# Optimization experiments

Hardware: AMD Instinct MI355X
Metric: run time of the kernel (lower is better)

## Reference

```python
import jax, jax.numpy as jnp
import numpy as np

N, E, IN = 50000, 800000, 64
HC, FC1, FC2, FC3, OUT = 96, 256, 128, 64, 8
EPS = 1e-5


def setup_inputs() -> dict:
    key = jax.random.key(0)
    ks = jax.random.split(key, 24)
    def lin(k, fi, fo):
        # kaiming_uniform with relu gain: bound = sqrt(6/fi)
        b = np.sqrt(6.0 / fi)
        return jax.random.uniform(k, (fi, fo), jnp.float32, -b, b)
    inp = {
        'x': jax.random.normal(ks[0], (N, IN), jnp.float32),
        'edge_index': jax.random.randint(ks[1], (2, E), 0, N, jnp.int64),
        'w1': lin(ks[2], IN, HC), 'b1': jnp.zeros((HC,), jnp.float32),
        'g1': jax.random.uniform(ks[3], (HC,), jnp.float32, 0.5, 1.5), 'be1': jax.random.normal(ks[4], (HC,), jnp.float32) * 0.1,
        'w2': lin(ks[5], HC, HC), 'b2': jnp.zeros((HC,), jnp.float32),
        'g2': jax.random.uniform(ks[6], (HC,), jnp.float32, 0.5, 1.5), 'be2': jax.random.normal(ks[7], (HC,), jnp.float32) * 0.1,
        'w3': lin(ks[8], HC, HC), 'b3': jnp.zeros((HC,), jnp.float32),
        'g3': jax.random.uniform(ks[9], (HC,), jnp.float32, 0.5, 1.5), 'be3': jax.random.normal(ks[10], (HC,), jnp.float32) * 0.1,
        'lw1': lin(ks[11], HC, FC1), 'lb1': jnp.zeros((FC1,), jnp.float32),
        'lw2': lin(ks[12], FC1, FC2), 'lb2': jnp.zeros((FC2,), jnp.float32),
        'lw3': lin(ks[13], FC2, FC3), 'lb3': jnp.zeros((FC3,), jnp.float32),
        'lw4': lin(ks[14], FC3, OUT), 'lb4': jnp.zeros((OUT,), jnp.float32),
    }
    return inp


def _gcn(x, w, b, src, dst, norm):
    # GCNConv: out[dst] += norm_e * (x @ w)[src]; then + bias
    h = x @ w
    msg = h[src] * norm[:, None]
    return jax.ops.segment_sum(msg, dst, num_segments=N) + b


def _bn_eval(x, g, be):
    # eval-mode BatchNorm1d with running_mean=0, running_var=1
    return x / jnp.sqrt(1.0 + EPS) * g + be


def reference(x, edge_index, w1, b1, g1, be1, w2, b2, g2, be2, w3, b3, g3, be3,
              lw1, lb1, lw2, lb2, lw3, lb3, lw4, lb4):
    loops = jnp.arange(N, dtype=edge_index.dtype)
    src = jnp.concatenate([edge_index[0], loops])
    dst = jnp.concatenate([edge_index[1], loops])
    deg = jax.ops.segment_sum(jnp.ones_like(src, jnp.float32), dst, num_segments=N)
    dinv = jax.lax.rsqrt(deg)  # deg >= 1 due to self loops
    norm = dinv[src] * dinv[dst]

    h = jax.nn.relu(_bn_eval(_gcn(x, w1, b1, src, dst, norm), g1, be1))
    h = jax.nn.relu(_bn_eval(_gcn(h, w2, b2, src, dst, norm), g2, be2))
    h = jax.nn.relu(_bn_eval(_gcn(h, w3, b3, src, dst, norm), g3, be3))
    h = jax.nn.relu(h @ lw1 + lb1)
    h = jax.nn.relu(h @ lw2 + lb2)
    h = jax.nn.relu(h @ lw3 + lb3)
    return h @ lw4 + lb4
```

## Files before the change

### kernel.cpp

```cpp
#include <hip/hip_runtime.h>


#define GN 50000
#define GE 800000
#define NPART 98
#define PSLOT 9216
#define CHK 2048

typedef __attribute__((ext_vector_type(8))) short bf16x8;
typedef __attribute__((ext_vector_type(4))) float floatx4;

__device__ __forceinline__ float ar1_b2f(unsigned short h) {
    return __uint_as_float(((unsigned)h) << 16);
}
__device__ __forceinline__ unsigned short ar1_f2b(float f) {
    unsigned u = __float_as_uint(f);
    u = u + 0x7FFFu + ((u >> 16) & 1u);
    return (unsigned short)(u >> 16);
}

__global__ void ar1_detect(const int* ei, const unsigned short* xw,
                           int* flagI, int* flagF, int* gcur) {
    __shared__ int cnt;
    if (threadIdx.x == 0) cnt = 0;
    __syncthreads();
    if (blockIdx.x == 0) {
        if ((int)threadIdx.x < NPART) gcur[threadIdx.x] = 0;
        if (ei[2 * threadIdx.x + 1] != 0) atomicAdd(&cnt, 1);
        __syncthreads();
        if (threadIdx.x == 0) flagI[0] = (cnt < 8) ? 1 : 0;
    } else {
        unsigned short w = xw[2 * threadIdx.x];
        int ex = (w >> 7) & 0xFF;
        if (w == 0 || (ex >= 90 && ex <= 150)) atomicAdd(&cnt, 1);
        __syncthreads();
        if (threadIdx.x == 0) flagF[0] = (cnt > 200) ? 0 : 1;
    }
}

__global__ __launch_bounds__(256)
void ar1_part(const int* __restrict__ ei, const int* __restrict__ flagI,
              int* __restrict__ gcur, unsigned int* __restrict__ pairs, int E) {
    __shared__ int cnt[NPART], base[NPART], cur[NPART];
    int tid = (int)threadIdx.x;
    for (int i = tid; i < NPART; i += 256) { cnt[i] = 0; cur[i] = 0; }
    __syncthreads();
    int is64 = flagI[0];
    int e0 = (int)blockIdx.x * CHK;
    unsigned pk[8]; int q[8];
#pragma unroll
    for (int k = 0; k < 8; k++) {
        int e = e0 + k * 256 + tid;
        q[k] = -1; pk[k] = 0;
        if (e < E) {
            int s = is64 ? ei[2 * e] : ei[e];
            int d = is64 ? ei[2 * (E + e)] : ei[E + e];
            if ((unsigned)s < (unsigned)GN && (unsigned)d < (unsigned)GN) {
                int qq = d >> 9;
                q[k] = qq;
                pk[k] = (unsigned)s | ((unsigned)(d & 511) << 17);
                atomicAdd(&cnt[qq], 1);
            }
        }
    }
    __syncthreads();
    for (int i = tid; i < NPART; i += 256)
        base[i] = (cnt[i] > 0) ? atomicAdd(&gcur[i], cnt[i]) : 0;
    __syncthreads();
#pragma unroll
    for (int k = 0; k < 8; k++) {
        if (q[k] >= 0) {
            int r = base[q[k]] + atomicAdd(&cur[q[k]], 1);
            if (r < PSLOT) pairs[(size_t)q[k] * PSLOT + r] = pk[k];
        }
    }
}

__global__ void ar1_pscan(const int* gcur, int* pbase) {
    __shared__ int sm[128];
    int tid = (int)threadIdx.x;
    int v = (tid < NPART) ? gcur[tid] : 0;
    sm[tid] = v;
    __syncthreads();
    for (int off = 1; off < 128; off <<= 1) {
        int t = (tid >= off) ? sm[tid - off] : 0;
        __syncthreads();
        sm[tid] += t;
        __syncthreads();
    }
    if (tid < NPART) pbase[tid] = sm[tid] - v;
}

__global__ __launch_bounds__(256)
void ar1_csr(const unsigned int* __restrict__ pairs, const int* __restrict__ gcur,
             const int* __restrict__ pbase, int* __restrict__ csr,
             int* __restrict__ indeg, int* __restrict__ offs,
             float* __restrict__ dinv) {
    __shared__ int ncnt[512], pre[512], cur[512], psum[16];
    int p = (int)blockIdx.x, tid = (int)threadIdx.x;
    int cntE = gcur[p];
    if (cntE > PSLOT) cntE = PSLOT;
    int gbase = pbase[p];
    for (int i = tid; i < 512; i += 256) ncnt[i] = 0;
    __syncthreads();
    const unsigned int* pp = pairs + (size_t)p * PSLOT;
    for (int i = tid; i < cntE; i += 256) atomicAdd(&ncnt[pp[i] >> 17], 1);
    __syncthreads();
    if (tid < 16) {
        int s = 0;
        for (int j = tid * 32; j < tid * 32 + 32; j++) { pre[j] = s; s += ncnt[j]; }
        psum[tid] = s;
    }
    __syncthreads();
    if (tid == 0) {
        int s = 0;
        for (int j = 0; j < 16; j++) { int t = psum[j]; psum[j] = s; s += t; }
    }
    __syncthreads();
    if (tid < 16)
        for (int j = tid * 32; j < tid * 32 + 32; j++) pre[j] += psum[tid];
    __syncthreads();
    for (int j = tid; j < 512; j += 256) {
        cur[j] = pre[j];
        int node = p * 512 + j;
        if (node < GN) {
            indeg[node] = ncnt[j];
            offs[node] = gbase + pre[j];
            dinv[node] = rsqrtf((float)(ncnt[j] + 1));
        }
    }
    __syncthreads();
    for (int i = tid; i < cntE; i += 256) {
        unsigned v = pp[i];
        int r = atomicAdd(&cur[v >> 17], 1);
        csr[gbase + r] = (int)(v & 0x1FFFFu);
    }
}

struct PackAll {
    const void* src[7];
    unsigned short* dst[7];
    int K[7], M[7], start[8];
};
struct SmallCvt {
    const void* src[4];
    float* dst[4];
    int n[4];
    const void* gb[9];
    float* ss[6];
};

__global__ void Arthur1_16458314678864_kernel(PackAll pa, SmallCvt sc,
                                              const int* flagF) {
    int b = (int)blockIdx.x;
    int f = flagF[0];
    if (b < 45) {
        int frag_g = b * 4 + ((int)threadIdx.x >> 6);
        if (frag_g >= 178) return;
        int w = 0;
        while (w < 6 && frag_g >= pa.start[w + 1]) w++;
        int frag = frag_g - pa.start[w];
        int K = pa.K[w], M = pa.M[w];
        int lane = (int)threadIdx.x & 63;
        int nch = K >> 5;
        int t = frag / nch, c = frag - t * nch;
        int n = t * 16 + (lane & 15);
        int k0 = c * 32 + (lane >> 4) * 8;
        unsigned short* o = pa.dst[w] + ((size_t)frag * 64 + lane) * 8;
        for (int j = 0; j < 8; j++) {
            unsigned short v = 0;
            if (n < M) {
                int idx = (k0 + j) * M + n;
                v = f ? ar1_f2b(((const float*)pa.src[w])[idx])
                      : ((const unsigned short*)pa.src[w])[idx];
            }
            o[j] = v;
        }
    } else {
        const float C = 0.9999950000374997f;
        for (int s = 0; s < 4; s++) {
            for (int i = threadIdx.x; i < sc.n[s]; i += 256) {
                float v = f ? ((const float*)sc.src[s])[i]
                            : ar1_b2f(((const unsigned short*)sc.src[s])[i]);
                sc.dst[s][i] = v;
            }
        }
        for (int k = 0; k < 3; k++) {
            for (int i = threadIdx.x; i < 96; i += 256) {
                float bb, g, be;
                if (f) {
                    bb = ((const float*)sc.gb[3 * k + 0])[i];
                    g  = ((const float*)sc.gb[3 * k + 1])[i];
                    be = ((const float*)sc.gb[3 * k + 2])[i];
                } else {
                    bb = ar1_b2f(((const unsigned short*)sc.gb[3 * k + 0])[i]);
                    g  = ar1_b2f(((const unsigned short*)sc.gb[3 * k + 1])[i]);
                    be = ar1_b2f(((const unsigned short*)sc.gb[3 * k + 2])[i]);
                }
                sc.ss[2 * k + 0][i] = C * g;
                sc.ss[2 * k + 1][i] = bb * C * g + be;
            }
        }
    }
}

template <int NT>
__global__ __launch_bounds__(256, 2)
void ar1_mfma(const unsigned short* __restrict__ A,
              const unsigned short* __restrict__ Bp,
              const float* __restrict__ scale, const float* __restrict__ shift,
              unsigned short* __restrict__ C, int K, int Astride, int Cstride) {
    int tid = (int)threadIdx.x;
    int wv = tid >> 6, lane = tid & 63;
    int mb = ((int)blockIdx.x * 4 + wv) * 16;
    int m = lane & 15, quad = lane >> 4;
    int arow = mb + m;
    if (arow >= GN) arow = GN - 1;
    const unsigned short* Aptr = A + (size_t)arow * Astride + quad * 8;
    int nch = K >> 5;

    floatx4 acc[NT];
#pragma unroll
    for (int t = 0; t < NT; t++) acc[t] = (floatx4){0.f, 0.f, 0.f, 0.f};

    for (int c = 0; c < nch; c++) {
        bf16x8 a = *((const bf16x8*)(Aptr + c * 32));
#pragma unroll
        for (int t = 0; t < NT; t++) {
            bf16x8 b = *((const bf16x8*)(Bp + ((size_t)(t * nch + c) * 64 + lane) * 8));
            acc[t] = __builtin_amdgcn_mfma_f32_16x16x32_bf16(a, b, acc[t], 0, 0, 0);
        }
    }

#pragma unroll
    for (int t = 0; t < NT; t++) {
#pragma unroll
        for (int r = 0; r < 4; r++) {
            int row = mb + quad * 4 + r;
            int col = t * 16 + m;
            if (row < GN) {
                float v = acc[t][r] * scale[col] + shift[col];
                C[(size_t)row * Cstride + col] = ar1_f2b(fmaxf(v, 0.f));
            }
        }
    }
}

__global__ __launch_bounds__(256, 2)
void ar1_mlp2(const unsigned short* __restrict__ A,
              const unsigned short* __restrict__ b2w,
              const float* __restrict__ sc3, const float* __restrict__ sh3,
              const unsigned short* __restrict__ b3,
              const unsigned short* __restrict__ b4,
              const unsigned short* __restrict__ b5,
              const unsigned short* __restrict__ b6,
              const float* __restrict__ lb0, const float* __restrict__ lb1,
              const float* __restrict__ lb2, const float* __restrict__ lb3,
              void* __restrict__ out, const int* __restrict__ f32out) {
    __shared__ unsigned short SH[16896 + 13312];
    unsigned short* H1 = SH;
    unsigned short* H0 = SH + 16896;
    unsigned short* H2 = SH + 16896;
    unsigned short* H3 = SH + 16896 + 8704;
    int tid = (int)threadIdx.x, wv = tid >> 6, lane = tid & 63;
    int m = lane & 15, quad = lane >> 4;
    int mb = (int)blockIdx.x * 64 + wv * 16;
    int lwv = wv * 16;

    {
        int arow = mb + m; if (arow >= GN) arow = GN - 1;
        const unsigned short* Ap = A + (size_t)arow * 96 + quad * 8;
        floatx4 acc[6];
#pragma unroll
        for (int t = 0; t < 6; t++) acc[t] = (floatx4){0.f, 0.f, 0.f, 0.f};
        for (int c = 0; c < 3; c++) {
            bf16x8 a = *((const bf16x8*)(Ap + c * 32));
#pragma unroll
            for (int t = 0; t < 6; t++) {
                bf16x8 b = *((const bf16x8*)(b2w + ((size_t)(t * 3 + c) * 64 + lane) * 8));
                acc[t] = __builtin_amdgcn_mfma_f32_16x16x32_bf16(a, b, acc[t], 0, 0, 0);
            }
        }
#pragma unroll
        for (int t = 0; t < 6; t++)
#pragma unroll
            for (int r = 0; r < 4; r++) {
                int lr = lwv + quad * 4 + r, col = t * 16 + m;
                float v = acc[t][r] * sc3[col] + sh3[col];
                H0[lr * 104 + col] = ar1_f2b(fmaxf(v, 0.f));
            }
    }
    {
        const unsigned short* Hp = H0 + (size_t)(lwv + m) * 104 + quad * 8;
        floatx4 acc[16];
#pragma unroll
        for (int t = 0; t < 16; t++) acc[t] = (floatx4){0.f, 0.f, 0.f, 0.f};
        for (int c = 0; c < 3; c++) {
            bf16x8 a = *((const bf16x8*)(Hp + c * 32));
#pragma unroll
            for (int t = 0; t < 16; t++) {
                bf16x8 b = *((const bf16x8*)(b3 + ((size_t)(t * 3 + c) * 64 + lane) * 8));
                acc[t] = __builtin_amdgcn_mfma_f32_16x16x32_bf16(a, b, acc[t], 0, 0, 0);
            }
        }
#pragma unroll
        for (int t = 0; t < 16; t++)
#pragma unroll
            for (int r = 0; r < 4; r++) {
                int lr = lwv + quad * 4 + r, col = t * 16 + m;
                H1[lr * 264 + col] = ar1_f2b(fmaxf(acc[t][r] + lb0[col], 0.f));
            }
    }
    {
        const unsigned short* Hp = H1 + (size_t)(lwv + m) * 264 + quad * 8;
        floatx4 acc[8];
#pragma unroll
        for (int t = 0; t < 8; t++) acc[t] = (floatx4){0.f, 0.f, 0.f, 0.f};
        for (int c = 0; c < 8; c++) {
            bf16x8 a = *((const bf16x8*)(Hp + c * 32));
#pragma unroll
            for (int t = 0; t < 8; t++) {
                bf16x8 b = *((const bf16x8*)(b4 + ((size_t)(t * 8 + c) * 64 + lane) * 8));
                acc[t] = __builtin_amdgcn_mfma_f32_16x16x32_bf16(a, b, acc[t], 0, 0, 0);
            }
        }
#pragma unroll
        for (int t = 0; t < 8; t++)
#pragma unroll
            for (int r = 0; r < 4; r++) {
                int lr = lwv + quad * 4 + r, col = t * 16 + m;
                H2[lr * 136 + col] = ar1_f2b(fmaxf(acc[t][r] + lb1[col], 0.f));
            }
    }
    {
        const unsigned short* Hp = H2 + (size_t)(lwv + m) * 136 + quad * 8;
        floatx4 acc[4];
#pragma unroll
        for (int t = 0; t < 4; t++) acc[t] = (floatx4){0.f, 0.f, 0.f, 0.f};
        for (int c = 0; c < 4; c++) {
            bf16x8 a = *((const bf16x8*)(Hp + c * 32));
#pragma unroll
            for (int t = 0; t < 4; t++) {
                bf16x8 b = *((const bf16x8*)(b5 + ((size_t)(t * 4 + c) * 64 + lane) * 8));
                acc[t] = __builtin_amdgcn_mfma_f32_16x16x32_bf16(a, b, acc[t], 0, 0, 0);
            }
        }
#pragma unroll
        for (int t = 0; t < 4; t++)
#pragma unroll
            for (int r = 0; r < 4; r++) {
                int lr = lwv + quad * 4 + r, col = t * 16 + m;
                H3[lr * 72 + col] = ar1_f2b(fmaxf(acc[t][r] + lb2[col], 0.f));
            }
    }
    {
        const unsigned short* Hp = H3 + (size_t)(lwv + m) * 72 + quad * 8;
        floatx4 acc = (floatx4){0.f, 0.f, 0.f, 0.f};
        for (int c = 0; c < 2; c++) {
            bf16x8 a = *((const bf16x8*)(Hp + c * 32));
            bf16x8 b = *((const bf16x8*)(b6 + ((size_t)c * 64 + lane) * 8));
            acc = __builtin_amdgcn_mfma_f32_16x16x32_bf16(a, b, acc, 0, 0, 0);
        }
        int wf32 = f32out[0];
#pragma unroll
        for (int r = 0; r < 4; r++) {
            int row = mb + quad * 4 + r;
            if (row < GN && m < 8) {
                float v = acc[r] + lb3[m];
                if (wf32) ((float*)out)[(size_t)row * 8 + m] = v;
                else ((unsigned short*)out)[(size_t)row * 8 + m] = ar1_f2b(v);
            }
        }
    }
}

__global__ __launch_bounds__(256, 8)
void ar1_agg64(const void* __restrict__ Xv, const int* __restrict__ offs,
               const int* __restrict__ indeg, const int* __restrict__ csr,
               const float* __restrict__ dinv, const int* __restrict__ flagF,
               unsigned short* __restrict__ Out) {
    int wv = (int)threadIdx.x >> 6, lane = (int)threadIdx.x & 63;
    int node = (int)blockIdx.x * 4 + wv;
    if (node >= GN) return;
    int chunk = lane & 7;
    int eslot = lane >> 3;
    float di = dinv[node];
    int off = offs[node], cnt = indeg[node];
    int f = flagF[0];
    const unsigned short* X16 = (const unsigned short*)Xv;
    const float* X32 = (const float*)Xv;

    float acc[8];
#pragma unroll
    for (int j = 0; j < 8; j++) acc[j] = 0.f;

    for (int base = 0; base < cnt; base += 16) {
        int ss[2]; float ww[2];
#pragma unroll
        for (int k = 0; k < 2; k++) {
            int e = base + k * 8 + eslot;
            int s = node; float w = 0.f;
            if (e < cnt) {
                s = csr[off + e];
                if ((unsigned)s >= (unsigned)GN) s = node;
                w = dinv[s] * di;
            }
            ss[k] = s; ww[k] = w;
        }
#pragma unroll
        for (int k = 0; k < 2; k++) {
            float hv[8];
            if (f) {
                floatx4 a = *((const floatx4*)(X32 + (size_t)ss[k] * 64 + chunk * 8));
                floatx4 b = *((const floatx4*)(X32 + (size_t)ss[k] * 64 + chunk * 8 + 4));
#pragma unroll
                for (int j = 0; j < 4; j++) { hv[j] = a[j]; hv[4 + j] = b[j]; }
            } else {
                bf16x8 h = *((const bf16x8*)(X16 + (size_t)ss[k] * 64 + chunk * 8));
#pragma unroll
                for (int j = 0; j < 8; j++) hv[j] = ar1_b2f((unsigned short)h[j]);
            }
#pragma unroll
            for (int j = 0; j < 8; j++) acc[j] += ww[k] * hv[j];
        }
    }

#pragma unroll
    for (int j = 0; j < 8; j++) {
        acc[j] += __shfl_xor(acc[j], 8, 64);
        acc[j] += __shfl_xor(acc[j], 16, 64);
        acc[j] += __shfl_xor(acc[j], 32, 64);
    }

    if (eslot == 0) {
        float hv[8];
        if (f) {
            floatx4 a = *((const floatx4*)(X32 + (size_t)node * 64 + chunk * 8));
            floatx4 b = *((const floatx4*)(X32 + (size_t)node * 64 + chunk * 8 + 4));
#pragma unroll
            for (int j = 0; j < 4; j++) { hv[j] = a[j]; hv[4 + j] = b[j]; }
        } else {
            bf16x8 h = *((const bf16x8*)(X16 + (size_t)node * 64 + chunk * 8));
#pragma unroll
            for (int j = 0; j < 8; j++) hv[j] = ar1_b2f((unsigned short)h[j]);
        }
#pragma unroll
        for (int j = 0; j < 8; j++) {
            float v = acc[j] + di * di * hv[j];
            Out[(size_t)node * 64 + chunk * 8 + j] = ar1_f2b(v);
        }
    }
}

__global__ __launch_bounds__(256, 8)
void ar1_agg96(const unsigned short* __restrict__ H, const int* __restrict__ offs,
               const int* __restrict__ indeg, const int* __restrict__ csr,
               const float* __restrict__ dinv, unsigned short* __restrict__ Out) {
    int wv = (int)threadIdx.x >> 6, lane = (int)threadIdx.x & 63;
    int node = (int)blockIdx.x * 4 + wv;
    if (node >= GN) return;
    int chunk = lane % 12;
    int eslot = lane / 12;
    int active = (lane < 48) ? 1 : 0;
    float di = dinv[node];
    int off = offs[node], cnt = indeg[node];

    float acc[8];
#pragma unroll
    for (int j = 0; j < 8; j++) acc[j] = 0.f;

    if (active) {
        for (int base = 0; base < cnt; base += 16) {
            int ss[4]; float ww[4]; bf16x8 hh[4];
#pragma unroll
            for (int k = 0; k < 4; k++) {
                int e = base + k * 4 + eslot;
                int s = node; float w = 0.f;
                if (e < cnt) {
                    s = csr[off + e];
                    if ((unsigned)s >= (unsigned)GN) s = node;
                    w = dinv[s] * di;
                }
                ss[k] = s; ww[k] = w;
            }
#pragma unroll
            for (int k = 0; k < 4; k++)
                hh[k] = *((const bf16x8*)(H + (size_t)ss[k] * 96 + chunk * 8));
#pragma unroll
            for (int k = 0; k < 4; k++)
#pragma unroll
                for (int j = 0; j < 8; j++)
                    acc[j] += ww[k] * ar1_b2f((unsigned short)hh[k][j]);
        }
    }

#pragma unroll
    for (int j = 0; j < 8; j++) {
        float a1 = __shfl(acc[j], lane + 12, 64);
        float a2 = __shfl(acc[j], lane + 24, 64);
        float a3 = __shfl(acc[j], lane + 36, 64);
        acc[j] += a1 + a2 + a3;
    }

    if (lane < 12) {
        bf16x8 hs = *((const bf16x8*)(H + (size_t)node * 96 + chunk * 8));
#pragma unroll
        for (int j = 0; j < 8; j++) {
            float v = acc[j] + di * di * ar1_b2f((unsigned short)hs[j]);
            Out[(size_t)node * 96 + chunk * 8 + j] = ar1_f2b(v);
        }
    }
}

extern "C" void kernel_launch(void* const* d_in, const int* in_sizes, int n_in,
                              void* d_out, int out_size, void* d_ws, size_t ws_size,
                              hipStream_t stream) {
    (void)in_sizes; (void)n_in; (void)out_size;

    char* p = (char*)d_ws;
    unsigned short* bufA = (unsigned short*)p; p += (size_t)GN * 96 * 2;
    unsigned short* bufC = (unsigned short*)p; p += (size_t)GN * 96 * 2;
    unsigned int* pairs = (unsigned int*)p; p += (size_t)NPART * PSLOT * 4;
    int* indeg  = (int*)p;    p += (size_t)GN * 4;
    int* offs   = (int*)p;    p += (size_t)GN * 4;
    float* dinv = (float*)p;  p += (size_t)GN * 4;
    int* csr    = (int*)p;    p += (size_t)GE * 4;
    int* gcur   = (int*)p;    p += 1024;
    int* pbase  = (int*)p;    p += 1024;
    int* flagI  = (int*)p;    p += 1024;
    int* flagF  = (int*)p;    p += 1024;
    unsigned short* bpArena = (unsigned short*)p; p += 91136 * 2;
    float* fArena = (float*)p; p += 2048 * 4;
    size_t need = (size_t)(p - (char*)d_ws);
    if (ws_size < need) {
        hipMemsetAsync(d_out, 0x41, (size_t)GN * 8 * 2, stream);
        return;
    }

    unsigned short* bp[7];
    int bpn[7] = {6144, 9216, 9216, 24576, 32768, 8192, 1024};
    {
        unsigned short* q = bpArena;
        for (int i = 0; i < 7; i++) { bp[i] = q; q += bpn[i]; }
    }

    float* lb[4]; float* ss[6];
    {
        float* q = fArena;
        int ln[4] = {256, 128, 64, 8};
        for (int i = 0; i < 4; i++) { lb[i] = q; q += ln[i]; }
        for (int i = 0; i < 6; i++) { ss[i] = q; q += 96; }
    }

    const int* ei = (const int*)d_in[1];

    ar1_detect<<<2, 256, 0, stream>>>(ei, (const unsigned short*)d_in[0], flagI, flagF, gcur);
    ar1_part<<<(GE + CHK - 1) / CHK, 256, 0, stream>>>(ei, flagI, gcur, pairs, GE);
    ar1_pscan<<<1, 128, 0, stream>>>(gcur, pbase);
    ar1_csr<<<NPART, 256, 0, stream>>>(pairs, gcur, pbase, csr, indeg, offs, dinv);

    {
        PackAll pa;
        int wsrc[7] = {2, 6, 10, 14, 16, 18, 20};
        int Ks[7] = {64, 96, 96, 96, 256, 128, 64};
        int Ms[7] = {96, 96, 96, 256, 128, 64, 8};
        int cum = 0;
        for (int i = 0; i < 7; i++) {
            pa.src[i] = d_in[wsrc[i]]; pa.dst[i] = bp[i];
            pa.K[i] = Ks[i]; pa.M[i] = Ms[i];
            pa.start[i] = cum;
            cum += (Ms[i] + 15) / 16 * (Ks[i] / 32);
        }
        pa.start[7] = cum;
        SmallCvt sc;
        int lsrc[4] = {15, 17, 19, 21};
        int ln[4] = {256, 128, 64, 8};
        for (int i = 0; i < 4; i++) { sc.src[i] = d_in[lsrc[i]]; sc.dst[i] = lb[i]; sc.n[i] = ln[i]; }
        int gsrc[9] = {3, 4, 5, 7, 8, 9, 11, 12, 13};
        for (int i = 0; i < 9; i++) sc.gb[i] = d_in[gsrc[i]];
        for (int i = 0; i < 6; i++) sc.ss[i] = ss[i];
        Arthur1_16458314678864_kernel<<<46, 256, 0, stream>>>(pa, sc, flagF);
    }

    const int GB = (GN + 63) / 64;
    const int AB = GN / 4;

    ar1_agg64<<<AB, 256, 0, stream>>>(d_in[0], offs, indeg, csr, dinv, flagF, bufC);
    ar1_mfma<6><<<GB, 256, 0, stream>>>(bufC, bp[0], ss[0], ss[1], bufA, 64, 64, 96);
    ar1_agg96<<<AB, 256, 0, stream>>>(bufA, offs, indeg, csr, dinv, bufC);
    ar1_mfma<6><<<GB, 256, 0, stream>>>(bufC, bp[1], ss[2], ss[3], bufA, 96, 96, 96);
    ar1_agg96<<<AB, 256, 0, stream>>>(bufA, offs, indeg, csr, dinv, bufC);

    ar1_mlp2<<<GB, 256, 0, stream>>>(bufC, bp[2], ss[4], ss[5],
                                     bp[3], bp[4], bp[5], bp[6],
                                     lb[0], lb[1], lb[2], lb[3], d_out, flagF);
}
```

Before: 312.6 us.

## Fuse graph aggregation with MFMA transform and merge preprocessing launches

Moves the detect, partition and weight-pack steps into one kernel launch. The partition blocks now detect the index dtype inline with wave shuffles, and the separate prefix-scan kernel becomes a per-block reduction inside the CSR kernel. The first two GCN layers now run aggregation and the 16-row MFMA matmul with BN/ReLU in a single 1024-thread kernel, staging aggregated rows in LDS. This removes several launches and an intermediate global round trip per layer, but adds an extra buffer and redundant flag detection in every block.

```diff
diff --git a/kernel.cpp b/kernel.cpp
--- a/kernel.cpp
+++ b/kernel.cpp
@@ -19,122 +19,30 @@
     return (unsigned short)(u >> 16);
 }
 
-__global__ void ar1_detect(const int* ei, const unsigned short* xw,
-                           int* flagI, int* flagF, int* gcur) {
-    __shared__ int cnt;
-    if (threadIdx.x == 0) cnt = 0;
-    __syncthreads();
-    if (blockIdx.x == 0) {
-        if ((int)threadIdx.x < NPART) gcur[threadIdx.x] = 0;
-        if (ei[2 * threadIdx.x + 1] != 0) atomicAdd(&cnt, 1);
-        __syncthreads();
-        if (threadIdx.x == 0) flagI[0] = (cnt < 8) ? 1 : 0;
-    } else {
-        unsigned short w = xw[2 * threadIdx.x];
+__device__ __forceinline__ int ar1_det64(const int* ei) {
+    int l = (int)threadIdx.x & 63;
+    int nz = 0;
+#pragma unroll
+    for (int k = 0; k < 4; k++)
+        nz += (ei[2 * (l + 64 * k) + 1] != 0) ? 1 : 0;
+#pragma unroll
+    for (int o = 1; o < 64; o <<= 1)
+        nz += __shfl_xor(nz, o, 64);
+    return (nz < 8) ? 1 : 0;
+}
+__device__ __forceinline__ int ar1_detf32(const unsigned short* xw) {
+    int l = (int)threadIdx.x & 63;
+    int c = 0;
+#pragma unroll
+    for (int k = 0; k < 4; k++) {
+        unsigned short w = xw[2 * (l + 64 * k)];
         int ex = (w >> 7) & 0xFF;
-        if (w == 0 || (ex >= 90 && ex <= 150)) atomicAdd(&cnt, 1);
-        __syncthreads();
-        if (threadIdx.x == 0) flagF[0] = (cnt > 200) ? 0 : 1;
-    }
-}
-
-__global__ __launch_bounds__(256)
-void ar1_part(const int* __restrict__ ei, const int* __restrict__ flagI,
-              int* __restrict__ gcur, unsigned int* __restrict__ pairs, int E) {
-    __shared__ int cnt[NPART], base[NPART], cur[NPART];
-    int tid = (int)threadIdx.x;
-    for (int i = tid; i < NPART; i += 256) { cnt[i] = 0; cur[i] = 0; }
-    __syncthreads();
-    int is64 = flagI[0];
-    int e0 = (int)blockIdx.x * CHK;
-    unsigned pk[8]; int q[8];
-#pragma unroll
-    for (int k = 0; k < 8; k++) {
-        int e = e0 + k * 256 + tid;
-        q[k] = -1; pk[k] = 0;
-        if (e < E) {
-            int s = is64 ? ei[2 * e] : ei[e];
-            int d = is64 ? ei[2 * (E + e)] : ei[E + e];
-            if ((unsigned)s < (unsigned)GN && (unsigned)d < (unsigned)GN) {
-                int qq = d >> 9;
-                q[k] = qq;
-                pk[k] = (unsigned)s | ((unsigned)(d & 511) << 17);
-                atomicAdd(&cnt[qq], 1);
-            }
-        }
-    }
-    __syncthreads();
-    for (int i = tid; i < NPART; i += 256)
-        base[i] = (cnt[i] > 0) ? atomicAdd(&gcur[i], cnt[i]) : 0;
-    __syncthreads();
-#pragma unroll
-    for (int k = 0; k < 8; k++) {
-        if (q[k] >= 0) {
-            int r = base[q[k]] + atomicAdd(&cur[q[k]], 1);
-            if (r < PSLOT) pairs[(size_t)q[k] * PSLOT + r] = pk[k];
-        }
-    }
-}
-
-__global__ void ar1_pscan(const int* gcur, int* pbase) {
-    __shared__ int sm[128];
-    int tid = (int)threadIdx.x;
-    int v = (tid < NPART) ? gcur[tid] : 0;
-    sm[tid] = v;
-    __syncthreads();
-    for (int off = 1; off < 128; off <<= 1) {
-        int t = (tid >= off) ? sm[tid - off] : 0;
-        __syncthreads();
-        sm[tid] += t;
-        __syncthreads();
-    }
-    if (tid < NPART) pbase[tid] = sm[tid] - v;
-}
-
-__global__ __launch_bounds__(256)
-void ar1_csr(const unsigned int* __restrict__ pairs, const int* __restrict__ gcur,
-             const int* __restrict__ pbase, int* __restrict__ csr,
-             int* __restrict__ indeg, int* __restrict__ offs,
-             float* __restrict__ dinv) {
-    __shared__ int ncnt[512], pre[512], cur[512], psum[16];
-    int p = (int)blockIdx.x, tid = (int)threadIdx.x;
-    int cntE = gcur[p];
-    if (cntE > PSLOT) cntE = PSLOT;
-    int gbase = pbase[p];
-    for (int i = tid; i < 512; i += 256) ncnt[i] = 0;
-    __syncthreads();
-    const unsigned int* pp = pairs + (size_t)p * PSLOT;
-    for (int i = tid; i < cntE; i += 256) atomicAdd(&ncnt[pp[i] >> 17], 1);
-    __syncthreads();
-    if (tid < 16) {
-        int s = 0;
-        for (int j = tid * 32; j < tid * 32 + 32; j++) { pre[j] = s; s += ncnt[j]; }
-        psum[tid] = s;
-    }
-    __syncthreads();
-    if (tid == 0) {
-        int s = 0;
-        for (int j = 0; j < 16; j++) { int t = psum[j]; psum[j] = s; s += t; }
-    }
-    __syncthreads();
-    if (tid < 16)
-        for (int j = tid * 32; j < tid * 32 + 32; j++) pre[j] += psum[tid];
-    __syncthreads();
-    for (int j = tid; j < 512; j += 256) {
-        cur[j] = pre[j];
-        int node = p * 512 + j;
-        if (node < GN) {
-            indeg[node] = ncnt[j];
-            offs[node] = gbase + pre[j];
-            dinv[node] = rsqrtf((float)(ncnt[j] + 1));
-        }
-    }
-    __syncthreads();
-    for (int i = tid; i < cntE; i += 256) {
-        unsigned v = pp[i];
-        int r = atomicAdd(&cur[v >> 17], 1);
-        csr[gbase + r] = (int)(v & 0x1FFFFu);
-    }
+        if (w == 0 || (ex >= 90 && ex <= 150)) c++;
+    }
+#pragma unroll
+    for (int o = 1; o < 64; o <<= 1)
+        c += __shfl_xor(c, o, 64);
+    return (c > 200) ? 0 : 1;
 }
 
 struct PackAll {
@@ -150,18 +58,57 @@
     float* ss[6];
 };
 
-__global__ void Arthur1_16458314678864_kernel(PackAll pa, SmallCvt sc,
-                                              const int* flagF) {
+__global__ __launch_bounds__(256)
+void Arthur1_16458314678864_kernel(PackAll pa, SmallCvt sc,
+                                   const int* __restrict__ ei,
+                                   const unsigned short* __restrict__ xw,
+                                   int* flagI, int* flagF,
+                                   int* __restrict__ gcur,
+                                   unsigned int* __restrict__ pairs) {
     int b = (int)blockIdx.x;
-    int f = flagF[0];
-    if (b < 45) {
-        int frag_g = b * 4 + ((int)threadIdx.x >> 6);
+    int tid = (int)threadIdx.x;
+    if (b < 391) {
+        __shared__ int cnt[NPART], base[NPART], cur[NPART];
+        for (int i = tid; i < NPART; i += 256) { cnt[i] = 0; cur[i] = 0; }
+        int is64 = ar1_det64(ei);
+        __syncthreads();
+        int e0 = b * CHK;
+        unsigned pk[8]; int q[8];
+#pragma unroll
+        for (int k = 0; k < 8; k++) {
+            int e = e0 + k * 256 + tid;
+            q[k] = -1; pk[k] = 0;
+            if (e < GE) {
+                int s = is64 ? ei[2 * e] : ei[e];
+                int d = is64 ? ei[2 * (GE + e)] : ei[GE + e];
+                if ((unsigned)s < (unsigned)GN && (unsigned)d < (unsigned)GN) {
+                    int qq = d >> 9;
+                    q[k] = qq;
+                    pk[k] = (unsigned)s | ((unsigned)(d & 511) << 17);
+                    atomicAdd(&cnt[qq], 1);
+                }
+            }
+        }
+        __syncthreads();
+        for (int i = tid; i < NPART; i += 256)
+            base[i] = (cnt[i] > 0) ? atomicAdd(&gcur[i], cnt[i]) : 0;
+        __syncthreads();
+#pragma unroll
+        for (int k = 0; k < 8; k++) {
+            if (q[k] >= 0) {
+                int r = base[q[k]] + atomicAdd(&cur[q[k]], 1);
+                if (r < PSLOT) pairs[(size_t)q[k] * PSLOT + r] = pk[k];
+            }
+        }
+    } else if (b < 436) {
+        int f = ar1_detf32(xw);
+        int frag_g = (b - 391) * 4 + (tid >> 6);
         if (frag_g >= 178) return;
         int w = 0;
         while (w < 6 && frag_g >= pa.start[w + 1]) w++;
         int frag = frag_g - pa.start[w];
         int K = pa.K[w], M = pa.M[w];
-        int lane = (int)threadIdx.x & 63;
+        int lane = tid & 63;
         int nch = K >> 5;
         int t = frag / nch, c = frag - t * nch;
         int n = t * 16 + (lane & 15);
@@ -177,16 +124,19 @@
             o[j] = v;
         }
     } else {
+        int f = ar1_detf32(xw);
+        int i64 = ar1_det64(ei);
+        if (tid == 0) { flagI[0] = i64; flagF[0] = f; }
         const float C = 0.9999950000374997f;
         for (int s = 0; s < 4; s++) {
-            for (int i = threadIdx.x; i < sc.n[s]; i += 256) {
+            for (int i = tid; i < sc.n[s]; i += 256) {
                 float v = f ? ((const float*)sc.src[s])[i]
                             : ar1_b2f(((const unsigned short*)sc.src[s])[i]);
                 sc.dst[s][i] = v;
             }
         }
         for (int k = 0; k < 3; k++) {
-            for (int i = threadIdx.x; i < 96; i += 256) {
+            for (int i = tid; i < 96; i += 256) {
                 float bb, g, be;
                 if (f) {
                     bb = ((const float*)sc.gb[3 * k + 0])[i];
@@ -204,44 +154,288 @@
     }
 }
 
-template <int NT>
-__global__ __launch_bounds__(256, 2)
-void ar1_mfma(const unsigned short* __restrict__ A,
-              const unsigned short* __restrict__ Bp,
-              const float* __restrict__ scale, const float* __restrict__ shift,
-              unsigned short* __restrict__ C, int K, int Astride, int Cstride) {
-    int tid = (int)threadIdx.x;
-    int wv = tid >> 6, lane = tid & 63;
-    int mb = ((int)blockIdx.x * 4 + wv) * 16;
-    int m = lane & 15, quad = lane >> 4;
-    int arow = mb + m;
-    if (arow >= GN) arow = GN - 1;
-    const unsigned short* Aptr = A + (size_t)arow * Astride + quad * 8;
-    int nch = K >> 5;
-
-    floatx4 acc[NT];
-#pragma unroll
-    for (int t = 0; t < NT; t++) acc[t] = (floatx4){0.f, 0.f, 0.f, 0.f};
-
-    for (int c = 0; c < nch; c++) {
-        bf16x8 a = *((const bf16x8*)(Aptr + c * 32));
-#pragma unroll
-        for (int t = 0; t < NT; t++) {
-            bf16x8 b = *((const bf16x8*)(Bp + ((size_t)(t * nch + c) * 64 + lane) * 8));
-            acc[t] = __builtin_amdgcn_mfma_f32_16x16x32_bf16(a, b, acc[t], 0, 0, 0);
-        }
-    }
-
-#pragma unroll
-    for (int t = 0; t < NT; t++) {
+__global__ __launch_bounds__(256)
+void ar1_csr(const unsigned int* __restrict__ pairs, const int* __restrict__ gcur,
+             int* __restrict__ csr, int* __restrict__ indeg,
+             int* __restrict__ offs, float* __restrict__ dinv) {
+    __shared__ int ncnt[512], pre[512], cur[512], psum[16], red[256];
+    int p = (int)blockIdx.x, tid = (int)threadIdx.x;
+    red[tid] = (tid < p && tid < NPART) ? gcur[tid] : 0;
+    __syncthreads();
+    for (int o = 128; o > 0; o >>= 1) {
+        if (tid < o) red[tid] += red[tid + o];
+        __syncthreads();
+    }
+    int gbase = red[0];
+    int cntE = gcur[p];
+    if (cntE > PSLOT) cntE = PSLOT;
+    for (int i = tid; i < 512; i += 256) ncnt[i] = 0;
+    __syncthreads();
+    const unsigned int* pp = pairs + (size_t)p * PSLOT;
+    for (int i = tid; i < cntE; i += 256) atomicAdd(&ncnt[pp[i] >> 17], 1);
+    __syncthreads();
+    if (tid < 16) {
+        int s = 0;
+        for (int j = tid * 32; j < tid * 32 + 32; j++) { pre[j] = s; s += ncnt[j]; }
+        psum[tid] = s;
+    }
+    __syncthreads();
+    if (tid == 0) {
+        int s = 0;
+        for (int j = 0; j < 16; j++) { int t = psum[j]; psum[j] = s; s += t; }
+    }
+    __syncthreads();
+    if (tid < 16)
+        for (int j = tid * 32; j < tid * 32 + 32; j++) pre[j] += psum[tid];
+    __syncthreads();
+    for (int j = tid; j < 512; j += 256) {
+        cur[j] = pre[j];
+        int node = p * 512 + j;
+        if (node < GN) {
+            indeg[node] = ncnt[j];
+            offs[node] = gbase + pre[j];
+            dinv[node] = rsqrtf((float)(ncnt[j] + 1));
+        }
+    }
+    __syncthreads();
+    for (int i = tid; i < cntE; i += 256) {
+        unsigned v = pp[i];
+        int r = atomicAdd(&cur[v >> 17], 1);
+        csr[gbase + r] = (int)(v & 0x1FFFFu);
+    }
+}
+
+__global__ __launch_bounds__(1024, 8)
+void ar1_ag64g(const void* __restrict__ Xv, const int* __restrict__ offs,
+               const int* __restrict__ indeg, const int* __restrict__ csr,
+               const float* __restrict__ dinv, const int* __restrict__ flagF,
+               const unsigned short* __restrict__ Bp,
+               const float* __restrict__ scale, const float* __restrict__ shift,
+               unsigned short* __restrict__ C) {
+    __shared__ unsigned short AL[16 * 72];
+    int tid = (int)threadIdx.x, wv = tid >> 6, lane = tid & 63;
+    int nb = (int)blockIdx.x * 16;
+    int node = nb + wv;
+    int chunk = lane & 7, eslot = lane >> 3;
+    int f = flagF[0];
+    const unsigned short* X16 = (const unsigned short*)Xv;
+    const float* X32 = (const float*)Xv;
+    float di = dinv[node];
+    int off = offs[node], cnt = indeg[node];
+
+    float acc[8];
+#pragma unroll
+    for (int j = 0; j < 8; j++) acc[j] = 0.f;
+
+    for (int base = 0; base < cnt; base += 16) {
+        int ss[2]; float ww[2];
+#pragma unroll
+        for (int k = 0; k < 2; k++) {
+            int e = base + k * 8 + eslot;
+            int s = node; float w = 0.f;
+            if (e < cnt) {
+                s = csr[off + e];
+                if ((unsigned)s >= (unsigned)GN) s = node;
+                w = dinv[s] * di;
+            }
+            ss[k] = s; ww[k] = w;
+        }
+#pragma unroll
+        for (int k = 0; k < 2; k++) {
+            float hv[8];
+            if (f) {
+                floatx4 a = *((const floatx4*)(X32 + (size_t)ss[k] * 64 + chunk * 8));
+                floatx4 b = *((const floatx4*)(X32 + (size_t)ss[k] * 64 + chunk * 8 + 4));
+#pragma unroll
+                for (int j = 0; j < 4; j++) { hv[j] = a[j]; hv[4 + j] = b[j]; }
+            } else {
+                bf16x8 h = *((const bf16x8*)(X16 + (size_t)ss[k] * 64 + chunk * 8));
+#pragma unroll
+                for (int j = 0; j < 8; j++) hv[j] = ar1_b2f((unsigned short)h[j]);
+            }
+#pragma unroll
+            for (int j = 0; j < 8; j++) acc[j] += ww[k] * hv[j];
+        }
+    }
+#pragma unroll
+    for (int j = 0; j < 8; j++) {
+        acc[j] += __shfl_xor(acc[j], 8, 64);
+        acc[j] += __shfl_xor(acc[j], 16, 64);
+        acc[j] += __shfl_xor(acc[j], 32, 64);
+    }
+    if (eslot == 0) {
+        float hv[8];
+        if (f) {
+            floatx4 a = *((const floatx4*)(X32 + (size_t)node * 64 + chunk * 8));
+            floatx4 b = *((const floatx4*)(X32 + (size_t)node * 64 + chunk * 8 + 4));
+#pragma unroll
+            for (int j = 0; j < 4; j++) { hv[j] = a[j]; hv[4 + j] = b[j]; }
+        } else {
+            bf16x8 h = *((const bf16x8*)(X16 + (size_t)node * 64 + chunk * 8));
+#pragma unroll
+            for (int j = 0; j < 8; j++) hv[j] = ar1_b2f((unsigned short)h[j]);
+        }
+        bf16x8 o;
+#pragma unroll
+        for (int j = 0; j < 8; j++)
+            o[j] = (short)ar1_f2b(acc[j] + di * di * hv[j]);
+        *((bf16x8*)(AL + (size_t)wv * 72 + chunk * 8)) = o;
+    }
+    __syncthreads();
+
+    if (wv < 6) {
+        int m = lane & 15, quad = lane >> 4, t = wv;
+        floatx4 g = (floatx4){0.f, 0.f, 0.f, 0.f};
+#pragma unroll
+        for (int c = 0; c < 2; c++) {
+            bf16x8 a = *((const bf16x8*)(AL + (size_t)m * 72 + c * 32 + quad * 8));
+            bf16x8 bfr = *((const bf16x8*)(Bp + ((size_t)(t * 2 + c) * 64 + lane) * 8));
+            g = __builtin_amdgcn_mfma_f32_16x16x32_bf16(a, bfr, g, 0, 0, 0);
+        }
 #pragma unroll
         for (int r = 0; r < 4; r++) {
-            int row = mb + quad * 4 + r;
+            int row = nb + quad * 4 + r;
             int col = t * 16 + m;
-            if (row < GN) {
-                float v = acc[t][r] * scale[col] + shift[col];
-                C[(size_t)row * Cstride + col] = ar1_f2b(fmaxf(v, 0.f));
-            }
+            float v = g[r] * scale[col] + shift[col];
+            C[(size_t)row * 96 + col] = ar1_f2b(fmaxf(v, 0.f));
+        }
+    }
+}
+
+__global__ __launch_bounds__(1024, 8)
+void ar1_ag96g(const unsigned short* __restrict__ H, const int* __restrict__ offs,
+               const int* __restrict__ indeg, const int* __restrict__ csr,
+               const float* __restrict__ dinv,
+               const unsigned short* __restrict__ Bp,
+               const float* __restrict__ scale, const float* __restrict__ shift,
+               unsigned short* __restrict__ C) {
+    __shared__ unsigned short AL[16 * 104];
+    int tid = (int)threadIdx.x, wv = tid >> 6, lane = tid & 63;
+    int nb = (int)blockIdx.x * 16;
+    int node = nb + wv;
+    int chunk = lane % 12, eslot = lane / 12;
+    int active = (lane < 48) ? 1 : 0;
+    float di = dinv[node];
+    int off = offs[node], cnt = indeg[node];
+
+    float acc[8];
+#pragma unroll
+    for (int j = 0; j < 8; j++) acc[j] = 0.f;
+
+    if (active) {
+        for (int base = 0; base < cnt; base += 16) {
+            int ss[4]; float ww[4]; bf16x8 hh[4];
+#pragma unroll
+            for (int k = 0; k < 4; k++) {
+                int e = base + k * 4 + eslot;
+                int s = node; float w = 0.f;
+                if (e < cnt) {
+                    s = csr[off + e];
+                    if ((unsigned)s >= (unsigned)GN) s = node;
+                    w = dinv[s] * di;
+                }
+                ss[k] = s; ww[k] = w;
+            }
+#pragma unroll
+            for (int k = 0; k < 4; k++)
+                hh[k] = *((const bf16x8*)(H + (size_t)ss[k] * 96 + chunk * 8));
+#pragma unroll
+            for (int k = 0; k < 4; k++)
+#pragma unroll
+                for (int j = 0; j < 8; j++)
+                    acc[j] += ww[k] * ar1_b2f((unsigned short)hh[k][j]);
+        }
+    }
+#pragma unroll
+    for (int j = 0; j < 8; j++) {
+        float a1 = __shfl(acc[j], lane + 12, 64);
+        float a2 = __shfl(acc[j], lane + 24, 64);
+        float a3 = __shfl(acc[j], lane + 36, 64);
+        acc[j] += a1 + a2 + a3;
+    }
+    if (lane < 12) {
+        bf16x8 hs = *((const bf16x8*)(H + (size_t)node * 96 + chunk * 8));
+        bf16x8 o;
+#pragma unroll
+        for (int j = 0; j < 8; j++)
+            o[j] = (short)ar1_f2b(acc[j] + di * di * ar1_b2f((unsigned short)hs[j]));
+        *((bf16x8*)(AL + (size_t)wv * 104 + chunk * 8)) = o;
+    }
+    __syncthreads();
+
+    if (wv < 6) {
+        int m = lane & 15, quad = lane >> 4, t = wv;
+        floatx4 g = (floatx4){0.f, 0.f, 0.f, 0.f};
+#pragma unroll
+        for (int c = 0; c < 3; c++) {
+            bf16x8 a = *((const bf16x8*)(AL + (size_t)m * 104 + c * 32 + quad * 8));
+            bf16x8 bfr = *((const bf16x8*)(Bp + ((size_t)(t * 3 + c) * 64 + lane) * 8));
+            g = __builtin_amdgcn_mfma_f32_16x16x32_bf16(a, bfr, g, 0, 0, 0);
+        }
+#pragma unroll
+        for (int r = 0; r < 4; r++) {
+            int row = nb + quad * 4 + r;
+            int col = t * 16 + m;
+            float v = g[r] * scale[col] + shift[col];
+            C[(size_t)row * 96 + col] = ar1_f2b(fmaxf(v, 0.f));
+        }
+    }
+}
+
+__global__ __launch_bounds__(256, 8)
+void ar1_agg96(const unsigned short* __restrict__ H, const int* __restrict__ offs,
+               const int* __restrict__ indeg, const int* __restrict__ csr,
+               const float* __restrict__ dinv, unsigned short* __restrict__ Out) {
+    int wv = (int)threadIdx.x >> 6, lane = (int)threadIdx.x & 63;
+    int node = (int)blockIdx.x * 4 + wv;
+    if (node >= GN) return;
+    int chunk = lane % 12;
+    int eslot = lane / 12;
+    int active = (lane < 48) ? 1 : 0;
+    float di = dinv[node];
+    int off = offs[node], cnt = indeg[node];
+
+    float acc[8];
+#pragma unroll
+    for (int j = 0; j < 8; j++) acc[j] = 0.f;
+
+    if (active) {
+        for (int base = 0; base < cnt; base += 16) {
+            int ss[4]; float ww[4]; bf16x8 hh[4];
+#pragma unroll
+            for (int k = 0; k < 4; k++) {
+                int e = base + k * 4 + eslot;
+                int s = node; float w = 0.f;
+                if (e < cnt) {
+                    s = csr[off + e];
+                    if ((unsigned)s >= (unsigned)GN) s = node;
+                    w = dinv[s] * di;
+                }
+                ss[k] = s; ww[k] = w;
+            }
+#pragma unroll
+            for (int k = 0; k < 4; k++)
+                hh[k] = *((const bf16x8*)(H + (size_t)ss[k] * 96 + chunk * 8));
+#pragma unroll
+            for (int k = 0; k < 4; k++)
+#pragma unroll
+                for (int j = 0; j < 8; j++)
+                    acc[j] += ww[k] * ar1_b2f((unsigned short)hh[k][j]);
+        }
+    }
+#pragma unroll
+    for (int j = 0; j < 8; j++) {
+        float a1 = __shfl(acc[j], lane + 12, 64);
+        float a2 = __shfl(acc[j], lane + 24, 64);
+        float a3 = __shfl(acc[j], lane + 36, 64);
+        acc[j] += a1 + a2 + a3;
+    }
+    if (lane < 12) {
+        bf16x8 hs = *((const bf16x8*)(H + (size_t)node * 96 + chunk * 8));
+#pragma unroll
+        for (int j = 0; j < 8; j++) {
+            float v = acc[j] + di * di * ar1_b2f((unsigned short)hs[j]);
+            Out[(size_t)node * 96 + chunk * 8 + j] = ar1_f2b(v);
         }
     }
 }
@@ -374,144 +568,6 @@
     }
 }
 
-__global__ __launch_bounds__(256, 8)
-void ar1_agg64(const void* __restrict__ Xv, const int* __restrict__ offs,
-               const int* __restrict__ indeg, const int* __restrict__ csr,
-               const float* __restrict__ dinv, const int* __restrict__ flagF,
-               unsigned short* __restrict__ Out) {
-    int wv = (int)threadIdx.x >> 6, lane = (int)threadIdx.x & 63;
-    int node = (int)blockIdx.x * 4 + wv;
-    if (node >= GN) return;
-    int chunk = lane & 7;
-    int eslot = lane >> 3;
-    float di = dinv[node];
-    int off = offs[node], cnt = indeg[node];
-    int f = flagF[0];
-    const unsigned short* X16 = (const unsigned short*)Xv;
-    const float* X32 = (const float*)Xv;
-
-    float acc[8];
-#pragma unroll
-    for (int j = 0; j < 8; j++) acc[j] = 0.f;
-
-    for (int base = 0; base < cnt; base += 16) {
-        int ss[2]; float ww[2];
-#pragma unroll
-        for (int k = 0; k < 2; k++) {
-            int e = base + k * 8 + eslot;
-            int s = node; float w = 0.f;
-            if (e < cnt) {
-                s = csr[off + e];
-                if ((unsigned)s >= (unsigned)GN) s = node;
-                w = dinv[s] * di;
-            }
-            ss[k] = s; ww[k] = w;
-        }
-#pragma unroll
-        for (int k = 0; k < 2; k++) {
-            float hv[8];
-            if (f) {
-                floatx4 a = *((const floatx4*)(X32 + (size_t)ss[k] * 64 + chunk * 8));
-                floatx4 b = *((const floatx4*)(X32 + (size_t)ss[k] * 64 + chunk * 8 + 4));
-#pragma unroll
-                for (int j = 0; j < 4; j++) { hv[j] = a[j]; hv[4 + j] = b[j]; }
-            } else {
-                bf16x8 h = *((const bf16x8*)(X16 + (size_t)ss[k] * 64 + chunk * 8));
-#pragma unroll
-                for (int j = 0; j < 8; j++) hv[j] = ar1_b2f((unsigned short)h[j]);
-            }
-#pragma unroll
-            for (int j = 0; j < 8; j++) acc[j] += ww[k] * hv[j];
-        }
-    }
-
-#pragma unroll
-    for (int j = 0; j < 8; j++) {
-        acc[j] += __shfl_xor(acc[j], 8, 64);
-        acc[j] += __shfl_xor(acc[j], 16, 64);
-        acc[j] += __shfl_xor(acc[j], 32, 64);
-    }
-
-    if (eslot == 0) {
-        float hv[8];
-        if (f) {
-            floatx4 a = *((const floatx4*)(X32 + (size_t)node * 64 + chunk * 8));
-            floatx4 b = *((const floatx4*)(X32 + (size_t)node * 64 + chunk * 8 + 4));
-#pragma unroll
-            for (int j = 0; j < 4; j++) { hv[j] = a[j]; hv[4 + j] = b[j]; }
-        } else {
-            bf16x8 h = *((const bf16x8*)(X16 + (size_t)node * 64 + chunk * 8));
-#pragma unroll
-            for (int j = 0; j < 8; j++) hv[j] = ar1_b2f((unsigned short)h[j]);
-        }
-#pragma unroll
-        for (int j = 0; j < 8; j++) {
-            float v = acc[j] + di * di * hv[j];
-            Out[(size_t)node * 64 + chunk * 8 + j] = ar1_f2b(v);
-        }
-    }
-}
-
-__global__ __launch_bounds__(256, 8)
-void ar1_agg96(const unsigned short* __restrict__ H, const int* __restrict__ offs,
-               const int* __restrict__ indeg, const int* __restrict__ csr,
-               const float* __restrict__ dinv, unsigned short* __restrict__ Out) {
-    int wv = (int)threadIdx.x >> 6, lane = (int)threadIdx.x & 63;
-    int node = (int)blockIdx.x * 4 + wv;
-    if (node >= GN) return;
-    int chunk = lane % 12;
-    int eslot = lane / 12;
-    int active = (lane < 48) ? 1 : 0;
-    float di = dinv[node];
-    int off = offs[node], cnt = indeg[node];
-
-    float acc[8];
-#pragma unroll
-    for (int j = 0; j < 8; j++) acc[j] = 0.f;
-
-    if (active) {
-        for (int base = 0; base < cnt; base += 16) {
-            int ss[4]; float ww[4]; bf16x8 hh[4];
-#pragma unroll
-            for (int k = 0; k < 4; k++) {
-                int e = base + k * 4 + eslot;
-                int s = node; float w = 0.f;
-                if (e < cnt) {
-                    s = csr[off + e];
-                    if ((unsigned)s >= (unsigned)GN) s = node;
-                    w = dinv[s] * di;
-                }
-                ss[k] = s; ww[k] = w;
-            }
-#pragma unroll
-            for (int k = 0; k < 4; k++)
-                hh[k] = *((const bf16x8*)(H + (size_t)ss[k] * 96 + chunk * 8));
-#pragma unroll
-            for (int k = 0; k < 4; k++)
-#pragma unroll
-                for (int j = 0; j < 8; j++)
-                    acc[j] += ww[k] * ar1_b2f((unsigned short)hh[k][j]);
-        }
-    }
-
-#pragma unroll
-    for (int j = 0; j < 8; j++) {
-        float a1 = __shfl(acc[j], lane + 12, 64);
-        float a2 = __shfl(acc[j], lane + 24, 64);
-        float a3 = __shfl(acc[j], lane + 36, 64);
-        acc[j] += a1 + a2 + a3;
-    }
-
-    if (lane < 12) {
-        bf16x8 hs = *((const bf16x8*)(H + (size_t)node * 96 + chunk * 8));
-#pragma unroll
-        for (int j = 0; j < 8; j++) {
-            float v = acc[j] + di * di * ar1_b2f((unsigned short)hs[j]);
-            Out[(size_t)node * 96 + chunk * 8 + j] = ar1_f2b(v);
-        }
-    }
-}
-
 extern "C" void kernel_launch(void* const* d_in, const int* in_sizes, int n_in,
                               void* d_out, int out_size, void* d_ws, size_t ws_size,
                               hipStream_t stream) {
@@ -519,6 +575,7 @@
 
     char* p = (char*)d_ws;
     unsigned short* bufA = (unsigned short*)p; p += (size_t)GN * 96 * 2;
+    unsigned short* bufB = (unsigned short*)p; p += (size_t)GN * 96 * 2;
     unsigned short* bufC = (unsigned short*)p; p += (size_t)GN * 96 * 2;
     unsigned int* pairs = (unsigned int*)p; p += (size_t)NPART * PSLOT * 4;
     int* indeg  = (int*)p;    p += (size_t)GN * 4;
@@ -526,7 +583,6 @@
     float* dinv = (float*)p;  p += (size_t)GN * 4;
     int* csr    = (int*)p;    p += (size_t)GE * 4;
     int* gcur   = (int*)p;    p += 1024;
-    int* pbase  = (int*)p;    p += 1024;
     int* flagI  = (int*)p;    p += 1024;
     int* flagF  = (int*)p;    p += 1024;
     unsigned short* bpArena = (unsigned short*)p; p += 91136 * 2;
@@ -553,12 +609,9 @@
     }
 
     const int* ei = (const int*)d_in[1];
-
-    ar1_detect<<<2, 256, 0, stream>>>(ei, (const unsigned short*)d_in[0], flagI, flagF, gcur);
-    ar1_part<<<(GE + CHK - 1) / CHK, 256, 0, stream>>>(ei, flagI, gcur, pairs, GE);
-    ar1_pscan<<<1, 128, 0, stream>>>(gcur, pbase);
-    ar1_csr<<<NPART, 256, 0, stream>>>(pairs, gcur, pbase, csr, indeg, offs, dinv);
-
+    const unsigned short* xw = (const unsigned short*)d_in[0];
+
+    hipMemsetAsync(gcur, 0, NPART * 4, stream);
     {
         PackAll pa;
         int wsrc[7] = {2, 6, 10, 14, 16, 18, 20};
@@ -579,17 +632,20 @@
         int gsrc[9] = {3, 4, 5, 7, 8, 9, 11, 12, 13};
         for (int i = 0; i < 9; i++) sc.gb[i] = d_in[gsrc[i]];
         for (int i = 0; i < 6; i++) sc.ss[i] = ss[i];
-        Arthur1_16458314678864_kernel<<<46, 256, 0, stream>>>(pa, sc, flagF);
-    }
+        Arthur1_16458314678864_kernel<<<437, 256, 0, stream>>>(
+            pa, sc, ei, xw, flagI, flagF, gcur, pairs);
+    }
+    ar1_csr<<<NPART, 256, 0, stream>>>(pairs, gcur, csr, indeg, offs, dinv);
 
     const int GB = (GN + 63) / 64;
     const int AB = GN / 4;
-
-    ar1_agg64<<<AB, 256, 0, stream>>>(d_in[0], offs, indeg, csr, dinv, flagF, bufC);
-    ar1_mfma<6><<<GB, 256, 0, stream>>>(bufC, bp[0], ss[0], ss[1], bufA, 64, 64, 96);
-    ar1_agg96<<<AB, 256, 0, stream>>>(bufA, offs, indeg, csr, dinv, bufC);
-    ar1_mfma<6><<<GB, 256, 0, stream>>>(bufC, bp[1], ss[2], ss[3], bufA, 96, 96, 96);
-    ar1_agg96<<<AB, 256, 0, stream>>>(bufA, offs, indeg, csr, dinv, bufC);
+    const int FB = GN / 16;
+
+    ar1_ag64g<<<FB, 1024, 0, stream>>>(d_in[0], offs, indeg, csr, dinv, flagF,
+                                       bp[0], ss[0], ss[1], bufA);
+    ar1_ag96g<<<FB, 1024, 0, stream>>>(bufA, offs, indeg, csr, dinv,
+                                       bp[1], ss[2], ss[3], bufB);
+    ar1_agg96<<<AB, 256, 0, stream>>>(bufB, offs, indeg, csr, dinv, bufC);
 
     ar1_mlp2<<<GB, 256, 0, stream>>>(bufC, bp[2], ss[4], ss[5],
                                      bp[3], bp[4], bp[5], bp[6],
```

New measurement: 292.8 us. 6.3% less time.
